# Optimization experiments

Hardware: AMD Instinct MI355X
Metric: run time of the kernel (lower is better)

## Reference

```python
import jax, jax.numpy as jnp
import numpy as np

N = 100000   # nodes
E = 1600000  # edges (avg degree 16)
D = 128      # feature dim (in_dim = out_dim = 128)


def setup_inputs() -> dict:
    key = jax.random.key(0)
    k0, k1, k2, k3, k4, k5 = jax.random.split(key, 6)
    x = jax.random.normal(k0, (N, D), dtype=jnp.float32)
    edge_index = jax.random.randint(k1, (2, E), 0, N, dtype=jnp.int32)
    # GCNConv linear weights (PyG stores lin.weight [out,in]; math is x @ W.T, here W:[in,out])
    s1 = 1.0 / np.sqrt(D)
    W1 = jax.random.uniform(k2, (D, D), jnp.float32, -s1, s1)
    b1 = jnp.zeros((D,), jnp.float32)
    W2 = jax.random.uniform(k3, (D, D), jnp.float32, -s1, s1)
    b2 = jnp.zeros((D,), jnp.float32)
    return {"x": x, "edge_index": edge_index, "W1": W1, "b1": b1, "W2": W2, "b2": b2}


def reference(x, edge_index, W1, b1, W2, b2):
    n = x.shape[0]
    idt = edge_index.dtype
    loop = jnp.arange(n, dtype=idt)
    src = jnp.concatenate([edge_index[0], loop])  # message sources
    dst = jnp.concatenate([edge_index[1], loop])  # aggregation targets
    # improved=True -> self-loop fill value 2.0; edge_weight=None -> ones
    w = jnp.concatenate([jnp.ones((edge_index.shape[1],), x.dtype),
                         jnp.full((n,), 2.0, x.dtype)])
    deg = jax.ops.segment_sum(w, dst, num_segments=n)
    dinv = jnp.where(deg > 0, jax.lax.rsqrt(deg), 0.0)
    norm = dinv[src] * w * dinv[dst]  # [E+N] symmetric GCN normalization

    def conv(h, W, b):
        h = h @ W  # [N, D] dense transform
        agg = jax.ops.segment_sum(norm[:, None] * h[src], dst, num_segments=n)
        return agg + b

    h = conv(x, W1, b1)        # conv1
    for _ in range(4):
        h = conv(h, W2, b2)
    return h
```

## Files before the change

### kernel.cpp

```cpp
#include <hip/hip_runtime.h>
#include <hip/hip_fp16.h>

#define D 128


__device__ inline float4 ld_h4(const __half* p) {
    float2 raw = *(const float2*)p;
    __half2 a = *reinterpret_cast<__half2*>(&raw.x);
    __half2 b = *reinterpret_cast<__half2*>(&raw.y);
    float2 fa = __half22float2(a), fb = __half22float2(b);
    return make_float4(fa.x, fa.y, fb.x, fb.y);
}

__device__ inline void unpack8(uint4 u, float* v) {
    const __half2* h = reinterpret_cast<const __half2*>(&u);
#pragma unroll
    for (int i = 0; i < 4; i++) {
        float2 f = __half22float2(h[i]);
        v[2 * i] = f.x; v[2 * i + 1] = f.y;
    }
}


__global__ void k_zero(int* __restrict__ p, int n) {
    int i = blockIdx.x * 256 + threadIdx.x;
    if (i < n) p[i] = 0;
}

__global__ void k_count(const int* __restrict__ dst, int* __restrict__ cnt,
                        int* __restrict__ rank, int e) {
    int i = blockIdx.x * 256 + threadIdx.x;
    if (i < e) rank[i] = atomicAdd(&cnt[dst[i]], 1);
}

__global__ void k_f2h(const float* __restrict__ in, __half* __restrict__ out, int n8) {
    int i = blockIdx.x * 256 + threadIdx.x;
    if (i < n8) {
        const float4* p = (const float4*)in + (size_t)i * 2;
        float4 a = p[0], b = p[1];
        __half2 h0 = __float22half2_rn(make_float2(a.x, a.y));
        __half2 h1 = __float22half2_rn(make_float2(a.z, a.w));
        __half2 h2 = __float22half2_rn(make_float2(b.x, b.y));
        __half2 h3 = __float22half2_rn(make_float2(b.z, b.w));
        uint4 o;
        o.x = *(unsigned*)&h0; o.y = *(unsigned*)&h1;
        o.z = *(unsigned*)&h2; o.w = *(unsigned*)&h3;
        ((uint4*)out)[i] = o;
    }
}


__global__ __launch_bounds__(256) void k_scanA(const int* __restrict__ cnt,
                                               int* __restrict__ partials,
                                               float* __restrict__ dinv, int n) {
    __shared__ int s[256];
    int b = blockIdx.x, t = threadIdx.x;
    int i0 = b * 512 + t * 2;
    int v = 0;
    if (i0 < n) {
        int c0 = cnt[i0];
        v += c0;
        dinv[i0] = 1.0f / sqrtf((float)(c0 + 2));
    }
    if (i0 + 1 < n) {
        int c1 = cnt[i0 + 1];
        v += c1;
        dinv[i0 + 1] = 1.0f / sqrtf((float)(c1 + 2));
    }
    s[t] = v;
    __syncthreads();
    for (int off = 128; off > 0; off >>= 1) {
        if (t < off) s[t] += s[t + off];
        __syncthreads();
    }
    if (t == 0) partials[b] = s[0];
}

__global__ __launch_bounds__(512) void k_scanB(const int* __restrict__ partials,
                                               int* __restrict__ base,
                                               int* __restrict__ off_n, int nb) {
    __shared__ int s[512];
    int t = threadIdx.x;
    int v = (t < nb) ? partials[t] : 0;
    s[t] = v;
    __syncthreads();
    for (int off = 1; off < 512; off <<= 1) {
        int x = (t >= off) ? s[t - off] : 0;
        __syncthreads();
        s[t] += x;
        __syncthreads();
    }
    if (t < nb) base[t] = s[t] - v;
    if (t == nb - 1) off_n[0] = s[t];
}

__global__ __launch_bounds__(256) void k_scanC(const int* __restrict__ cnt,
                                               const int* __restrict__ base,
                                               int* __restrict__ offsets, int n) {
    __shared__ int s[256];
    int b = blockIdx.x, t = threadIdx.x;
    int i0 = b * 512 + t * 2;
    int v0 = (i0 < n) ? cnt[i0] : 0;
    int v1 = (i0 + 1 < n) ? cnt[i0 + 1] : 0;
    int sum = v0 + v1;
    s[t] = sum;
    __syncthreads();
    for (int off = 1; off < 256; off <<= 1) {
        int x = (t >= off) ? s[t - off] : 0;
        __syncthreads();
        s[t] += x;
        __syncthreads();
    }
    int excl = s[t] - sum + base[b];
    if (i0 < n) offsets[i0] = excl;
    if (i0 + 1 < n) offsets[i0 + 1] = excl + v0;
}

__global__ void k_fill(const int* __restrict__ src, const int* __restrict__ dst,
                       const int* __restrict__ rank, const int* __restrict__ offsets,
                       const float* __restrict__ dinv, int2* __restrict__ csr, int e) {
    int i = blockIdx.x * 256 + threadIdx.x;
    if (i < e) {
        int s = src[i];
        int d = dst[i];
        int pos = offsets[d] + rank[i];
        csr[pos] = make_int2(s, __float_as_int(dinv[s] * dinv[d]));
    }
}

__global__ __launch_bounds__(128) void k_wmm(const float* __restrict__ A,
                                             const float* __restrict__ B,
                                             float* __restrict__ Cm) {
    __shared__ float a[128];
    int r = blockIdx.x, d = threadIdx.x;
    a[d] = A[r * 128 + d];
    __syncthreads();
    float acc = 0.0f;
#pragma unroll 8
    for (int k = 0; k < 128; k++) acc += a[k] * B[k * 128 + d];
    Cm[r * 128 + d] = acc;
}

__global__ __launch_bounds__(128) void k_wmm_bias(const float* __restrict__ W1,
                                                  const float* __restrict__ W4,
                                                  const float* __restrict__ W2,
                                                  const float* __restrict__ b1,
                                                  const float* __restrict__ b2,
                                                  float* __restrict__ Wtot,
                                                  float* __restrict__ cmat) {
    __shared__ float s[128];
    int d = threadIdx.x;
    if (blockIdx.x < 128) {
        int r = blockIdx.x;
        s[d] = W1[r * 128 + d];
        __syncthreads();
        float acc = 0.0f;
#pragma unroll 8
        for (int k = 0; k < 128; k++) acc += s[k] * W4[k * 128 + d];
        Wtot[r * 128 + d] = acc;
        return;
    }
    float v = b2[d];
    cmat[d] = v;
    for (int j = 1; j <= 3; j++) {
        s[d] = v;
        __syncthreads();
        float acc = 0.0f;
#pragma unroll 8
        for (int k = 0; k < 128; k++) acc += s[k] * W2[k * 128 + d];
        v = acc;
        cmat[j * 128 + d] = v;
        __syncthreads();
    }
    s[d] = b1[d];
    __syncthreads();
    float acc = 0.0f;
#pragma unroll 8
    for (int k = 0; k < 128; k++) acc += s[k] * W4[k * 128 + d];
    cmat[4 * 128 + d] = acc;
}

__global__ __launch_bounds__(256) void k_matmul(const __half* __restrict__ Hh,
                                                const float* __restrict__ W,
                                                float* __restrict__ O,
                                                const float* __restrict__ ucol,
                                                const float* __restrict__ cmat,
                                                int nrows) {
    __shared__ float Ws[32 * D];
    __shared__ float HsT[32 * 128];
    const int t = threadIdx.x;
    const int row0 = blockIdx.x * 128;
    const int tx = t & 15;
    const int ty = t >> 4;
    const int r_st = t & 127;
    const int kb = (t >> 7) * 16;
    const int gr = row0 + r_st;
    const bool grok = (gr < nrows);

    float acc[8][8];
    {
        float bc[8];
#pragma unroll
        for (int j = 0; j < 8; j++) bc[j] = cmat[tx * 8 + j];
#pragma unroll
        for (int i = 0; i < 8; i++)
#pragma unroll
            for (int j = 0; j < 8; j++) acc[i][j] = bc[j];
    }
#pragma unroll
    for (int tt = 0; tt < 4; tt++) {
        float c0 = cmat[(tt + 1) * D + tx * 8 + 0], c1 = cmat[(tt + 1) * D + tx * 8 + 1];
        float c2 = cmat[(tt + 1) * D + tx * 8 + 2], c3 = cmat[(tt + 1) * D + tx * 8 + 3];
        float c4 = cmat[(tt + 1) * D + tx * 8 + 4], c5 = cmat[(tt + 1) * D + tx * 8 + 5];
        float c6 = cmat[(tt + 1) * D + tx * 8 + 6], c7 = cmat[(tt + 1) * D + tx * 8 + 7];
#pragma unroll
        for (int i = 0; i < 8; i++) {
            int gr2 = row0 + ty * 8 + i;
            if (gr2 < nrows) {
                float ut = ucol[(size_t)tt * nrows + gr2];
                acc[i][0] += ut * c0; acc[i][1] += ut * c1;
                acc[i][2] += ut * c2; acc[i][3] += ut * c3;
                acc[i][4] += ut * c4; acc[i][5] += ut * c5;
                acc[i][6] += ut * c6; acc[i][7] += ut * c7;
            }
        }
    }

    float4 w0, w1, w2, w3;
    uint4 hp0, hp1;
    {
        const float4* W4p = (const float4*)W;
        w0 = W4p[t]; w1 = W4p[t + 256]; w2 = W4p[t + 512]; w3 = W4p[t + 768];
        if (grok) {
            const uint4* Hp = (const uint4*)(Hh + (size_t)gr * D + kb);
            hp0 = Hp[0]; hp1 = Hp[1];
        } else {
            hp0 = hp1 = make_uint4(0, 0, 0, 0);
        }
    }

    for (int kc = 0; kc < D; kc += 32) {
        {
            float4* Ws4 = (float4*)Ws;
            Ws4[t] = w0; Ws4[t + 256] = w1; Ws4[t + 512] = w2; Ws4[t + 768] = w3;
            float vals[16];
            unpack8(hp0, vals);
            unpack8(hp1, vals + 8);
#pragma unroll
            for (int j = 0; j < 16; j++) HsT[(kb + j) * 128 + r_st] = vals[j];
        }
        __syncthreads();

        if (kc + 32 < D) {
            const float4* W4p = (const float4*)(W + (kc + 32) * D);
            w0 = W4p[t]; w1 = W4p[t + 256]; w2 = W4p[t + 512]; w3 = W4p[t + 768];
            if (grok) {
                const uint4* Hp = (const uint4*)(Hh + (size_t)gr * D + (kc + 32) + kb);
                hp0 = Hp[0]; hp1 = Hp[1];
            }
        }

#pragma unroll 8
        for (int k = 0; k < 32; k++) {
            float4 a0 = *(const float4*)&HsT[k * 128 + ty * 8];
            float4 a1 = *(const float4*)&HsT[k * 128 + ty * 8 + 4];
            float4 b0 = *(const float4*)&Ws[k * D + tx * 8];
            float4 b1 = *(const float4*)&Ws[k * D + tx * 8 + 4];
            float ar[8] = {a0.x, a0.y, a0.z, a0.w, a1.x, a1.y, a1.z, a1.w};
            float br[8] = {b0.x, b0.y, b0.z, b0.w, b1.x, b1.y, b1.z, b1.w};
#pragma unroll
            for (int i = 0; i < 8; i++)
#pragma unroll
                for (int j = 0; j < 8; j++) acc[i][j] += ar[i] * br[j];
        }
        __syncthreads();
    }
#pragma unroll
    for (int i = 0; i < 8; i++) {
        int gr2 = row0 + ty * 8 + i;
        if (gr2 < nrows) {
            float4* Op = (float4*)(O + (size_t)gr2 * D + tx * 8);
            Op[0] = make_float4(acc[i][0], acc[i][1], acc[i][2], acc[i][3]);
            Op[1] = make_float4(acc[i][4], acc[i][5], acc[i][6], acc[i][7]);
        }
    }
}

template <bool WITH_U, bool IN_F16, bool OUT_F16>
__global__ __launch_bounds__(256) void k_gather(const void* __restrict__ Tv,
                                                const int2* __restrict__ csr,
                                                const int* __restrict__ offsets,
                                                const float* __restrict__ dinv,
                                                void* __restrict__ Ov,
                                                const float* __restrict__ uin,
                                                float* __restrict__ uout, int n) {
    int node = blockIdx.x * 4 + (threadIdx.x >> 6);
    if (node >= n) return;
    int lane = threadIdx.x & 63;
    int hf = lane >> 5;
    int c = (lane & 31) << 2;
    const __half* Tch = (const __half*)Tv + c;
    const float*  Tcf = (const float*)Tv + c;

    float ax = 0.f, ay = 0.f, az = 0.f, aw = 0.f;
    float uacc = 0.f;
    if (hf == 0) {
        float di = dinv[node];
        float sw = 2.0f * di * di;
        float4 v = IN_F16 ? ld_h4(Tch + (size_t)node * D)
                          : *(const float4*)(Tcf + (size_t)node * D);
        ax = sw * v.x; ay = sw * v.y; az = sw * v.z; aw = sw * v.w;
        if (WITH_U) uacc = sw * (uin ? uin[node] : 1.0f);
    }

    int e = offsets[node];
    const int e1 = offsets[node + 1];

    for (; e + 8 <= e1; e += 8) {
        int2 p0 = csr[e + hf];
        int2 p1 = csr[e + 2 + hf];
        int2 p2 = csr[e + 4 + hf];
        int2 p3 = csr[e + 6 + hf];
        float4 v0, v1, v2, v3;
        if (IN_F16) {
            v0 = ld_h4(Tch + (size_t)p0.x * D);
            v1 = ld_h4(Tch + (size_t)p1.x * D);
            v2 = ld_h4(Tch + (size_t)p2.x * D);
            v3 = ld_h4(Tch + (size_t)p3.x * D);
        } else {
            v0 = *(const float4*)(Tcf + (size_t)p0.x * D);
            v1 = *(const float4*)(Tcf + (size_t)p1.x * D);
            v2 = *(const float4*)(Tcf + (size_t)p2.x * D);
            v3 = *(const float4*)(Tcf + (size_t)p3.x * D);
        }
        float w0 = __int_as_float(p0.y), w1 = __int_as_float(p1.y);
        float w2 = __int_as_float(p2.y), w3 = __int_as_float(p3.y);
        if (WITH_U) {
            if (uin) {
                uacc += w0 * uin[p0.x] + w1 * uin[p1.x]
                      + w2 * uin[p2.x] + w3 * uin[p3.x];
            } else {
                uacc += w0 + w1 + w2 + w3;
            }
        }
        ax += w0 * v0.x; ay += w0 * v0.y; az += w0 * v0.z; aw += w0 * v0.w;
        ax += w1 * v1.x; ay += w1 * v1.y; az += w1 * v1.z; aw += w1 * v1.w;
        ax += w2 * v2.x; ay += w2 * v2.y; az += w2 * v2.z; aw += w2 * v2.w;
        ax += w3 * v3.x; ay += w3 * v3.y; az += w3 * v3.z; aw += w3 * v3.w;
    }
    for (; e + 2 <= e1; e += 2) {
        int2 p0 = csr[e + hf];
        float4 v0 = IN_F16 ? ld_h4(Tch + (size_t)p0.x * D)
                           : *(const float4*)(Tcf + (size_t)p0.x * D);
        float w0 = __int_as_float(p0.y);
        if (WITH_U) uacc += w0 * (uin ? uin[p0.x] : 1.0f);
        ax += w0 * v0.x; ay += w0 * v0.y; az += w0 * v0.z; aw += w0 * v0.w;
    }
    if (e < e1 && hf == 0) {
        int2 p0 = csr[e];
        float4 v0 = IN_F16 ? ld_h4(Tch + (size_t)p0.x * D)
                           : *(const float4*)(Tcf + (size_t)p0.x * D);
        float w0 = __int_as_float(p0.y);
        if (WITH_U) uacc += w0 * (uin ? uin[p0.x] : 1.0f);
        ax += w0 * v0.x; ay += w0 * v0.y; az += w0 * v0.z; aw += w0 * v0.w;
    }

    ax += __shfl_xor(ax, 32, 64);
    ay += __shfl_xor(ay, 32, 64);
    az += __shfl_xor(az, 32, 64);
    aw += __shfl_xor(aw, 32, 64);
    if (WITH_U) uacc += __shfl_xor(uacc, 32, 64);

    if (hf == 0) {
        if (OUT_F16) {
            __half2 o01 = __float22half2_rn(make_float2(ax, ay));
            __half2 o23 = __float22half2_rn(make_float2(az, aw));
            float2 raw;
            *(__half2*)&raw.x = o01;
            *(__half2*)&raw.y = o23;
            *(float2*)((__half*)Ov + (size_t)node * D + c) = raw;
        } else {
            *(float4*)((float*)Ov + (size_t)node * D + c) =
                make_float4(ax, ay, az, aw);
        }
        if (WITH_U && lane == 0) uout[node] = uacc;
    }
}


extern "C" void kernel_launch(void* const* d_in, const int* in_sizes, int n_in,
                              void* d_out, int out_size, void* d_ws, size_t ws_size,
                              hipStream_t stream) {
    const float* x  = (const float*)d_in[0];
    const int*   ei = (const int*)d_in[1];
    const float* W1 = (const float*)d_in[2];
    const float* b1 = (const float*)d_in[3];
    const float* W2 = (const float*)d_in[4];
    const float* b2 = (const float*)d_in[5];
    const int N = in_sizes[0] / D;
    const int E = in_sizes[1] / 2;
    float* out = (float*)d_out;

    char* ws = (char*)d_ws;
    size_t woff = 0;
    auto alloc = [&](size_t bytes) -> void* {
        void* p = ws + woff;
        woff = (woff + bytes + 15) & ~(size_t)15;
        return p;
    };
    __half* T16a    = (__half*)alloc((size_t)N * D * sizeof(__half));
    __half* T16b    = (__half*)alloc((size_t)N * D * sizeof(__half));
    int*   cnt      = (int*)  alloc((size_t)N * sizeof(int));
    int*   offsets  = (int*)  alloc((size_t)(N + 1) * sizeof(int));
    int*   rank     = (int*)  alloc((size_t)E * sizeof(int));
    float* dinv     = (float*)alloc((size_t)N * sizeof(float));
    int2*  csr      = (int2*) alloc((size_t)E * sizeof(int2));
    int*   partials = (int*)  alloc(1024 * sizeof(int));
    int*   base     = (int*)  alloc(1024 * sizeof(int));
    float* ucol     = (float*)alloc((size_t)4 * N * sizeof(float));
    float* cmat     = (float*)alloc(5 * 128 * sizeof(float));
    float* Wsq      = (float*)alloc(128 * 128 * sizeof(float));
    float* W4       = (float*)alloc(128 * 128 * sizeof(float));
    float* Wtot     = (float*)alloc(128 * 128 * sizeof(float));
    size_t x16_bytes = (size_t)N * D * sizeof(__half);
    bool use_x16 = (woff + x16_bytes) <= ws_size;
    __half* X16 = use_x16 ? (__half*)alloc(x16_bytes) : nullptr;
    (void)n_in; (void)out_size;

    const int* e_src = ei;
    const int* e_dst = ei + E;
    const int NB = (N + 511) / 512;

    k_zero<<<(N + 255) / 256, 256, 0, stream>>>(cnt, N);
    k_count<<<(E + 255) / 256, 256, 0, stream>>>(e_dst, cnt, rank, E);
    k_scanA<<<NB, 256, 0, stream>>>(cnt, partials, dinv, N);
    k_scanB<<<1, 512, 0, stream>>>(partials, base, offsets + N, NB);
    k_scanC<<<NB, 256, 0, stream>>>(cnt, base, offsets, N);
    k_fill<<<(E + 255) / 256, 256, 0, stream>>>(e_src, e_dst, rank, offsets,
                                                dinv, csr, E);

    const int GG = (N + 3) / 4;
    if (use_x16) {
        int n8 = (N * D) / 8;
        k_f2h<<<(n8 + 255) / 256, 256, 0, stream>>>(x, X16, n8);
        k_gather<true, true, true><<<GG, 256, 0, stream>>>(
            X16, csr, offsets, dinv, T16a, nullptr, ucol, N);
    } else {
        k_gather<true, false, true><<<GG, 256, 0, stream>>>(
            x, csr, offsets, dinv, T16a, nullptr, ucol, N);
    }
    k_gather<true,  true, true><<<GG, 256, 0, stream>>>(
        T16a, csr, offsets, dinv, T16b, ucol,         ucol + N,     N);
    k_gather<true,  true, true><<<GG, 256, 0, stream>>>(
        T16b, csr, offsets, dinv, T16a, ucol + N,     ucol + 2 * N, N);
    k_gather<true,  true, true><<<GG, 256, 0, stream>>>(
        T16a, csr, offsets, dinv, T16b, ucol + 2 * N, ucol + 3 * N, N);
    k_gather<false, true, true><<<GG, 256, 0, stream>>>(
        T16b, csr, offsets, dinv, T16a, nullptr,      nullptr,      N);

    k_wmm<<<128, 128, 0, stream>>>(W2, W2, Wsq);
    k_wmm<<<128, 128, 0, stream>>>(Wsq, Wsq, W4);
    k_wmm_bias<<<129, 128, 0, stream>>>(W1, W4, W2, b1, b2, Wtot, cmat);

    k_matmul<<<(N + 127) / 128, 256, 0, stream>>>(T16a, Wtot, out, ucol, cmat, N);
}
```

Baseline: 689.6 us.

## Use MFMA f16 matrix cores with split-half weights for final matmul

Replaces the FP32 shared-memory tiled matmul with a per-wave MFMA 16x16x32 f16 kernel. The combined weight matrix is pre-packed into a high half plus a residual half, so two MFMAs per tile keep near-FP32 weight accuracy. The kernel now reads weights straight from global memory in MFMA fragment layout and no longer stages through LDS. The gather kernels also switch to direct half-to-float FMA accumulation, which is a minor change. Output stores are scalar and strided per lane, which may cost write efficiency.

```diff
diff --git a/kernel.cpp b/kernel.cpp
--- a/kernel.cpp
+++ b/kernel.cpp
@@ -3,22 +3,18 @@
 
 #define D 128
 
-
-__device__ inline float4 ld_h4(const __half* p) {
-    float2 raw = *(const float2*)p;
-    __half2 a = *reinterpret_cast<__half2*>(&raw.x);
-    __half2 b = *reinterpret_cast<__half2*>(&raw.y);
-    float2 fa = __half22float2(a), fb = __half22float2(b);
-    return make_float4(fa.x, fa.y, fb.x, fb.y);
-}
-
-__device__ inline void unpack8(uint4 u, float* v) {
-    const __half2* h = reinterpret_cast<const __half2*>(&u);
-#pragma unroll
-    for (int i = 0; i < 4; i++) {
-        float2 f = __half22float2(h[i]);
-        v[2 * i] = f.x; v[2 * i + 1] = f.y;
-    }
+typedef _Float16 half8 __attribute__((ext_vector_type(8)));
+typedef float floatx4 __attribute__((ext_vector_type(4)));
+
+
+__device__ inline void acc_h4(float& ax, float& ay, float& az, float& aw,
+                              float w, uint2 raw) {
+    __half2 h01 = *reinterpret_cast<const __half2*>(&raw.x);
+    __half2 h23 = *reinterpret_cast<const __half2*>(&raw.y);
+    ax = fmaf(w, __low2float(h01), ax);
+    ay = fmaf(w, __high2float(h01), ay);
+    az = fmaf(w, __low2float(h23), az);
+    aw = fmaf(w, __high2float(h23), aw);
 }
 
 
@@ -180,108 +176,79 @@
     cmat[4 * 128 + d] = acc;
 }
 
+__global__ __launch_bounds__(256) void k_wpack(const float* __restrict__ Wtot,
+                                               __half* __restrict__ pack) {
+    int tid = blockIdx.x * 256 + threadIdx.x;
+    int l = tid & 63, t = (tid >> 6) & 7, s = tid >> 9;
+    int col = t * 16 + (l & 15);
+    int krow = s * 32 + 8 * (l >> 4);
+#pragma unroll
+    for (int j = 0; j < 8; j++) {
+        float w = Wtot[(krow + j) * 128 + col];
+        __half hh = __float2half(w);
+        float rem = w - __half2float(hh);
+        pack[(size_t)tid * 8 + j] = hh;
+        pack[16384 + (size_t)tid * 8 + j] = __float2half(rem);
+    }
+}
+
 __global__ __launch_bounds__(256) void k_matmul(const __half* __restrict__ Hh,
-                                                const float* __restrict__ W,
+                                                const __half* __restrict__ Wpack,
                                                 float* __restrict__ O,
                                                 const float* __restrict__ ucol,
                                                 const float* __restrict__ cmat,
                                                 int nrows) {
-    __shared__ float Ws[32 * D];
-    __shared__ float HsT[32 * 128];
     const int t = threadIdx.x;
-    const int row0 = blockIdx.x * 128;
-    const int tx = t & 15;
-    const int ty = t >> 4;
-    const int r_st = t & 127;
-    const int kb = (t >> 7) * 16;
-    const int gr = row0 + r_st;
-    const bool grok = (gr < nrows);
-
-    float acc[8][8];
-    {
-        float bc[8];
-#pragma unroll
-        for (int j = 0; j < 8; j++) bc[j] = cmat[tx * 8 + j];
-#pragma unroll
-        for (int i = 0; i < 8; i++)
-#pragma unroll
-            for (int j = 0; j < 8; j++) acc[i][j] = bc[j];
-    }
-#pragma unroll
-    for (int tt = 0; tt < 4; tt++) {
-        float c0 = cmat[(tt + 1) * D + tx * 8 + 0], c1 = cmat[(tt + 1) * D + tx * 8 + 1];
-        float c2 = cmat[(tt + 1) * D + tx * 8 + 2], c3 = cmat[(tt + 1) * D + tx * 8 + 3];
-        float c4 = cmat[(tt + 1) * D + tx * 8 + 4], c5 = cmat[(tt + 1) * D + tx * 8 + 5];
-        float c6 = cmat[(tt + 1) * D + tx * 8 + 6], c7 = cmat[(tt + 1) * D + tx * 8 + 7];
-#pragma unroll
-        for (int i = 0; i < 8; i++) {
-            int gr2 = row0 + ty * 8 + i;
-            if (gr2 < nrows) {
-                float ut = ucol[(size_t)tt * nrows + gr2];
-                acc[i][0] += ut * c0; acc[i][1] += ut * c1;
-                acc[i][2] += ut * c2; acc[i][3] += ut * c3;
-                acc[i][4] += ut * c4; acc[i][5] += ut * c5;
-                acc[i][6] += ut * c6; acc[i][7] += ut * c7;
-            }
-        }
-    }
-
-    float4 w0, w1, w2, w3;
-    uint4 hp0, hp1;
-    {
-        const float4* W4p = (const float4*)W;
-        w0 = W4p[t]; w1 = W4p[t + 256]; w2 = W4p[t + 512]; w3 = W4p[t + 768];
-        if (grok) {
-            const uint4* Hp = (const uint4*)(Hh + (size_t)gr * D + kb);
-            hp0 = Hp[0]; hp1 = Hp[1];
-        } else {
-            hp0 = hp1 = make_uint4(0, 0, 0, 0);
-        }
-    }
-
-    for (int kc = 0; kc < D; kc += 32) {
-        {
-            float4* Ws4 = (float4*)Ws;
-            Ws4[t] = w0; Ws4[t + 256] = w1; Ws4[t + 512] = w2; Ws4[t + 768] = w3;
-            float vals[16];
-            unpack8(hp0, vals);
-            unpack8(hp1, vals + 8);
-#pragma unroll
-            for (int j = 0; j < 16; j++) HsT[(kb + j) * 128 + r_st] = vals[j];
-        }
-        __syncthreads();
-
-        if (kc + 32 < D) {
-            const float4* W4p = (const float4*)(W + (kc + 32) * D);
-            w0 = W4p[t]; w1 = W4p[t + 256]; w2 = W4p[t + 512]; w3 = W4p[t + 768];
-            if (grok) {
-                const uint4* Hp = (const uint4*)(Hh + (size_t)gr * D + (kc + 32) + kb);
-                hp0 = Hp[0]; hp1 = Hp[1];
-            }
-        }
-
-#pragma unroll 8
-        for (int k = 0; k < 32; k++) {
-            float4 a0 = *(const float4*)&HsT[k * 128 + ty * 8];
-            float4 a1 = *(const float4*)&HsT[k * 128 + ty * 8 + 4];
-            float4 b0 = *(const float4*)&Ws[k * D + tx * 8];
-            float4 b1 = *(const float4*)&Ws[k * D + tx * 8 + 4];
-            float ar[8] = {a0.x, a0.y, a0.z, a0.w, a1.x, a1.y, a1.z, a1.w};
-            float br[8] = {b0.x, b0.y, b0.z, b0.w, b1.x, b1.y, b1.z, b1.w};
-#pragma unroll
-            for (int i = 0; i < 8; i++)
-#pragma unroll
-                for (int j = 0; j < 8; j++) acc[i][j] += ar[i] * br[j];
-        }
-        __syncthreads();
-    }
-#pragma unroll
-    for (int i = 0; i < 8; i++) {
-        int gr2 = row0 + ty * 8 + i;
-        if (gr2 < nrows) {
-            float4* Op = (float4*)(O + (size_t)gr2 * D + tx * 8);
-            Op[0] = make_float4(acc[i][0], acc[i][1], acc[i][2], acc[i][3]);
-            Op[1] = make_float4(acc[i][4], acc[i][5], acc[i][6], acc[i][7]);
+    const int lane = t & 63, wave = t >> 6;
+    const int rows0 = blockIdx.x * 64 + wave * 16;
+    const int lrow = lane & 15, lk = lane >> 4;
+
+    float uu[4][4];
+#pragma unroll
+    for (int r = 0; r < 4; r++) {
+        int row = rows0 + lk * 4 + r;
+        if (row >= nrows) row = nrows - 1;
+#pragma unroll
+        for (int tt = 0; tt < 4; tt++) uu[tt][r] = ucol[(size_t)tt * nrows + row];
+    }
+
+    floatx4 acc[8];
+#pragma unroll
+    for (int tl = 0; tl < 8; tl++) {
+        int col = tl * 16 + lrow;
+        float c0 = cmat[col];
+        float c1 = cmat[128 + col], c2 = cmat[256 + col];
+        float c3 = cmat[384 + col], c4 = cmat[512 + col];
+#pragma unroll
+        for (int r = 0; r < 4; r++)
+            acc[tl][r] = c0 + uu[0][r] * c1 + uu[1][r] * c2
+                            + uu[2][r] * c3 + uu[3][r] * c4;
+    }
+
+    int arow = rows0 + lrow;
+    if (arow >= nrows) arow = nrows - 1;
+    const __half* abase = Hh + (size_t)arow * 128 + lk * 8;
+
+#pragma unroll
+    for (int s = 0; s < 4; s++) {
+        half8 a = *reinterpret_cast<const half8*>(abase + s * 32);
+        const __half* wb = Wpack + (size_t)s * 4096 + (size_t)lane * 8;
+#pragma unroll
+        for (int tl = 0; tl < 8; tl++) {
+            half8 bh = *reinterpret_cast<const half8*>(wb + (size_t)tl * 512);
+            half8 bl = *reinterpret_cast<const half8*>(wb + (size_t)tl * 512 + 16384);
+            acc[tl] = __builtin_amdgcn_mfma_f32_16x16x32_f16(a, bh, acc[tl], 0, 0, 0);
+            acc[tl] = __builtin_amdgcn_mfma_f32_16x16x32_f16(a, bl, acc[tl], 0, 0, 0);
+        }
+    }
+
+#pragma unroll
+    for (int r = 0; r < 4; r++) {
+        int row = rows0 + lk * 4 + r;
+        if (row < nrows) {
+            float* orow = O + (size_t)row * 128 + lrow;
+#pragma unroll
+            for (int tl = 0; tl < 8; tl++) orow[tl * 16] = acc[tl][r];
         }
     }
 }
@@ -307,9 +274,13 @@
     if (hf == 0) {
         float di = dinv[node];
         float sw = 2.0f * di * di;
-        float4 v = IN_F16 ? ld_h4(Tch + (size_t)node * D)
-                          : *(const float4*)(Tcf + (size_t)node * D);
-        ax = sw * v.x; ay = sw * v.y; az = sw * v.z; aw = sw * v.w;
+        if (IN_F16) {
+            uint2 raw = *(const uint2*)(Tch + (size_t)node * D);
+            acc_h4(ax, ay, az, aw, sw, raw);
+        } else {
+            float4 v = *(const float4*)(Tcf + (size_t)node * D);
+            ax = sw * v.x; ay = sw * v.y; az = sw * v.z; aw = sw * v.w;
+        }
         if (WITH_U) uacc = sw * (uin ? uin[node] : 1.0f);
     }
 
@@ -321,48 +292,67 @@
         int2 p1 = csr[e + 2 + hf];
         int2 p2 = csr[e + 4 + hf];
         int2 p3 = csr[e + 6 + hf];
-        float4 v0, v1, v2, v3;
-        if (IN_F16) {
-            v0 = ld_h4(Tch + (size_t)p0.x * D);
-            v1 = ld_h4(Tch + (size_t)p1.x * D);
-            v2 = ld_h4(Tch + (size_t)p2.x * D);
-            v3 = ld_h4(Tch + (size_t)p3.x * D);
-        } else {
-            v0 = *(const float4*)(Tcf + (size_t)p0.x * D);
-            v1 = *(const float4*)(Tcf + (size_t)p1.x * D);
-            v2 = *(const float4*)(Tcf + (size_t)p2.x * D);
-            v3 = *(const float4*)(Tcf + (size_t)p3.x * D);
-        }
         float w0 = __int_as_float(p0.y), w1 = __int_as_float(p1.y);
         float w2 = __int_as_float(p2.y), w3 = __int_as_float(p3.y);
-        if (WITH_U) {
-            if (uin) {
-                uacc += w0 * uin[p0.x] + w1 * uin[p1.x]
-                      + w2 * uin[p2.x] + w3 * uin[p3.x];
-            } else {
-                uacc += w0 + w1 + w2 + w3;
+        if (IN_F16) {
+            uint2 r0 = *(const uint2*)(Tch + (size_t)p0.x * D);
+            uint2 r1 = *(const uint2*)(Tch + (size_t)p1.x * D);
+            uint2 r2 = *(const uint2*)(Tch + (size_t)p2.x * D);
+            uint2 r3 = *(const uint2*)(Tch + (size_t)p3.x * D);
+            if (WITH_U) {
+                if (uin) {
+                    uacc += w0 * uin[p0.x] + w1 * uin[p1.x]
+                          + w2 * uin[p2.x] + w3 * uin[p3.x];
+                } else {
+                    uacc += w0 + w1 + w2 + w3;
+                }
             }
-        }
-        ax += w0 * v0.x; ay += w0 * v0.y; az += w0 * v0.z; aw += w0 * v0.w;
-        ax += w1 * v1.x; ay += w1 * v1.y; az += w1 * v1.z; aw += w1 * v1.w;
-        ax += w2 * v2.x; ay += w2 * v2.y; az += w2 * v2.z; aw += w2 * v2.w;
-        ax += w3 * v3.x; ay += w3 * v3.y; az += w3 * v3.z; aw += w3 * v3.w;
+            acc_h4(ax, ay, az, aw, w0, r0);
+            acc_h4(ax, ay, az, aw, w1, r1);
+            acc_h4(ax, ay, az, aw, w2, r2);
+            acc_h4(ax, ay, az, aw, w3, r3);
+        } else {
+            float4 v0 = *(const float4*)(Tcf + (size_t)p0.x * D);
+            float4 v1 = *(const float4*)(Tcf + (size_t)p1.x * D);
+            float4 v2 = *(const float4*)(Tcf + (size_t)p2.x * D);
+            float4 v3 = *(const float4*)(Tcf + (size_t)p3.x * D);
+            if (WITH_U) {
+                if (uin) {
+                    uacc += w0 * uin[p0.x] + w1 * uin[p1.x]
+                          + w2 * uin[p2.x] + w3 * uin[p3.x];
+                } else {
+                    uacc += w0 + w1 + w2 + w3;
+                }
+            }
+            ax += w0 * v0.x; ay += w0 * v0.y; az += w0 * v0.z; aw += w0 * v0.w;
+            ax += w1 * v1.x; ay += w1 * v1.y; az += w1 * v1.z; aw += w1 * v1.w;
+            ax += w2 * v2.x; ay += w2 * v2.y; az += w2 * v2.z; aw += w2 * v2.w;
+            ax += w3 * v3.x; ay += w3 * v3.y; az += w3 * v3.z; aw += w3 * v3.w;
+        }
     }
     for (; e + 2 <= e1; e += 2) {
         int2 p0 = csr[e + hf];
-        float4 v0 = IN_F16 ? ld_h4(Tch + (size_t)p0.x * D)
-                           : *(const float4*)(Tcf + (size_t)p0.x * D);
         float w0 = __int_as_float(p0.y);
         if (WITH_U) uacc += w0 * (uin ? uin[p0.x] : 1.0f);
-        ax += w0 * v0.x; ay += w0 * v0.y; az += w0 * v0.z; aw += w0 * v0.w;
+        if (IN_F16) {
+            uint2 r0 = *(const uint2*)(Tch + (size_t)p0.x * D);
+            acc_h4(ax, ay, az, aw, w0, r0);
+        } else {
+            float4 v0 = *(const float4*)(Tcf + (size_t)p0.x * D);
+            ax += w0 * v0.x; ay += w0 * v0.y; az += w0 * v0.z; aw += w0 * v0.w;
+        }
     }
     if (e < e1 && hf == 0) {
         int2 p0 = csr[e];
-        float4 v0 = IN_F16 ? ld_h4(Tch + (size_t)p0.x * D)
-                           : *(const float4*)(Tcf + (size_t)p0.x * D);
         float w0 = __int_as_float(p0.y);
         if (WITH_U) uacc += w0 * (uin ? uin[p0.x] : 1.0f);
-        ax += w0 * v0.x; ay += w0 * v0.y; az += w0 * v0.z; aw += w0 * v0.w;
+        if (IN_F16) {
+            uint2 r0 = *(const uint2*)(Tch + (size_t)p0.x * D);
+            acc_h4(ax, ay, az, aw, w0, r0);
+        } else {
+            float4 v0 = *(const float4*)(Tcf + (size_t)p0.x * D);
+            ax += w0 * v0.x; ay += w0 * v0.y; az += w0 * v0.z; aw += w0 * v0.w;
+        }
     }
 
     ax += __shfl_xor(ax, 32, 64);
@@ -420,8 +410,9 @@
     float* ucol     = (float*)alloc((size_t)4 * N * sizeof(float));
     float* cmat     = (float*)alloc(5 * 128 * sizeof(float));
     float* Wsq      = (float*)alloc(128 * 128 * sizeof(float));
-    float* W4       = (float*)alloc(128 * 128 * sizeof(float));
+    float* W4      = (float*)alloc(128 * 128 * sizeof(float));
     float* Wtot     = (float*)alloc(128 * 128 * sizeof(float));
+    __half* Wpack   = (__half*)alloc(32768 * sizeof(__half));
     size_t x16_bytes = (size_t)N * D * sizeof(__half);
     bool use_x16 = (woff + x16_bytes) <= ws_size;
     __half* X16 = use_x16 ? (__half*)alloc(x16_bytes) : nullptr;
@@ -461,6 +452,7 @@
     k_wmm<<<128, 128, 0, stream>>>(W2, W2, Wsq);
     k_wmm<<<128, 128, 0, stream>>>(Wsq, Wsq, W4);
     k_wmm_bias<<<129, 128, 0, stream>>>(W1, W4, W2, b1, b2, Wtot, cmat);
-
-    k_matmul<<<(N + 127) / 128, 256, 0, stream>>>(T16a, Wtot, out, ucol, cmat, N);
-}
+    k_wpack<<<8, 256, 0, stream>>>(Wtot, Wpack);
+
+    k_matmul<<<(N + 63) / 64, 256, 0, stream>>>(T16a, Wpack, out, ucol, cmat, N);
+}
```

After: 658.2 us. 4.6% less time.
